# Performance work log

Measured on AMD Instinct MI355X. Metric: run time of the kernel, lower is better.

Reference implementation:

```python
import jax, jax.numpy as jnp
import numpy as np

B, L, D, H = 2, 2048, 1024, 16
DH = D // H
NEG = -10000.0

def setup_inputs() -> dict:
    key = jax.random.key(0)
    ks = jax.random.split(key, 6)
    scale = 1.0 / np.sqrt(D)
    inp = {
        "x": jax.random.normal(ks[0], (B, L, D), dtype=jnp.float32),
        "m": jnp.ones((B, L), dtype=jnp.int32),  # 1 = valid token, 0 = padded
        "Wq": jax.random.normal(ks[1], (D, D), dtype=jnp.float32) * scale,
        "bq": jnp.zeros((D,), dtype=jnp.float32),
        "Wk": jax.random.normal(ks[2], (D, D), dtype=jnp.float32) * scale,
        "bk": jnp.zeros((D,), dtype=jnp.float32),
        "Wv": jax.random.normal(ks[3], (D, D), dtype=jnp.float32) * scale,
        "bv": jnp.zeros((D,), dtype=jnp.float32),
        "Wp": jax.random.normal(ks[4], (D, D), dtype=jnp.float32) * scale,
        "bp": jnp.zeros((D,), dtype=jnp.float32),
    }
    return inp

def reference(x, m, Wq, bq, Wk, bk, Wv, bv, Wp, bp):
    # torch Linear: x @ W.T + b
    def heads(t):  # (B,L,D) -> (B,H,L,DH)
        return t.reshape(B, L, H, DH).transpose(0, 2, 1, 3)
    q = heads(x @ Wq.T + bq)
    k = heads(x @ Wk.T + bk)
    v = heads(x @ Wv.T + bv)
    att = jnp.einsum("bhqd,bhkd->bhqk", q, k) * (1.0 / np.sqrt(DH))  # (B,H,L,L)
    causal = jnp.tril(jnp.ones((L, L), dtype=bool))[None, None]       # (1,1,L,L)
    att = jnp.where(causal, att, NEG)
    # additive key-padding mask: 0 for valid, -10000 for padded keys
    pad = (1.0 - m.astype(att.dtype))[:, None, None, :] * NEG         # (B,1,1,L)
    att = att + pad
    att = jax.nn.softmax(att, axis=-1)
    y = jnp.einsum("bhqk,bhkd->bhqd", att, v)                          # (B,H,L,DH)
    y = y.transpose(0, 2, 1, 3).reshape(B, L, D)
    return y @ Wp.T + bp
```

## Files before the change

kernel.cpp:

```cpp
#include <hip/hip_runtime.h>
#include <hip/hip_bf16.h>

#define NB 2
#define NL 2048
#define ND 1024
#define NH 16
#define NDH 64
#define NM (NB*NL)

typedef unsigned short u16;
typedef __attribute__((ext_vector_type(8))) short short8;
typedef __attribute__((ext_vector_type(4))) float floatx4;

#define QSCALE 0.180336880f

__device__ __forceinline__ float bf2f(u16 u) {
  union { unsigned int ui; float f; } w;
  w.ui = ((unsigned int)u) << 16;
  return w.f;
}

__device__ __forceinline__ u16 f2bf(float f) {
  union { float f; unsigned int u; } v; v.f = f;
  unsigned int r = v.u + 0x7FFF + ((v.u >> 16) & 1);
  return (u16)(r >> 16);
}

__device__ __forceinline__ void async_cp16(const u16* lds, const u16* g) {
  __builtin_amdgcn_global_load_lds(
      (const __attribute__((address_space(1))) void*)g,
      (__attribute__((address_space(3))) void*)lds, 16, 0, 0);
}

__device__ __forceinline__ float dpp_xor1_f(float v) {
  return __int_as_float(__builtin_amdgcn_mov_dpp(__float_as_int(v), 0xB1, 0xF, 0xF, true));
}

__device__ __forceinline__ unsigned pk_bf16(float lo, float hi) {
  __hip_bfloat162 h2 = __float22bfloat162_rn(make_float2(lo, hi));
  return *(unsigned*)&h2;
}

__global__ __launch_bounds__(256)
void cvt_all(const float* __restrict__ wq, const float* __restrict__ wk,
             const float* __restrict__ wv, const float* __restrict__ wp,
             const float* __restrict__ x,
             u16* __restrict__ ow, u16* __restrict__ ox)
{
  const int per4 = ND * ND / 4;
  const int tot  = 4 * per4 + NM * ND / 4;
  for (int t = blockIdx.x * 256 + threadIdx.x; t < tot; t += gridDim.x * 256) {
    const float* src; uint2* dst; int off;
    if (t < 4 * per4) {
      int w = t >> 18; off = t & (per4 - 1);
      src = (w == 0) ? wq : (w == 1) ? wk : (w == 2) ? wv : wp;
      dst = (uint2*)(ow + (size_t)w * ND * ND);
    } else {
      off = t - 4 * per4; src = x; dst = (uint2*)ox;
    }
    float4 f = ((const float4*)src)[off];
    u16 h[4] = { f2bf(f.x), f2bf(f.y), f2bf(f.z), f2bf(f.w) };
    dst[off] = *(const uint2*)h;
  }
}

#define BM 128
#define BN 128
#define BK 32
#define LDT 32

__global__ __launch_bounds__(256)
void gemm_qkv(const u16* __restrict__ A, const u16* __restrict__ Wb,
              const float* __restrict__ bq, const float* __restrict__ bk,
              const float* __restrict__ bv,
              u16* __restrict__ Qb, u16* __restrict__ Kb, u16* __restrict__ Vb)
{
  const int n0g = blockIdx.x * BN;
  const int z   = n0g >> 10;
  const int n0  = n0g & 1023;
  const u16* W    = Wb + (size_t)z * ND * ND;
  const float* Bi = (z == 0) ? bq : (z == 1) ? bk : bv;
  u16* C          = (z == 0) ? Qb : (z == 1) ? Kb : Vb;
  const float sc  = (z == 0) ? QSCALE : 1.0f;

  const int m0 = blockIdx.y * BM;
  const int tid  = threadIdx.x;
  const int lane = tid & 63;
  const int wave = tid >> 6;
  const int wm = (wave >> 1) * 64;
  const int wn = (wave & 1) * 64;
  const int quad = lane >> 4;
  const int l16  = lane & 15;

  __shared__ u16 As[BM * LDT];
  __shared__ u16 Bs[BN * LDT];

  floatx4 acc[4][4];
#pragma unroll
  for (int i = 0; i < 4; ++i)
#pragma unroll
    for (int j = 0; j < 4; ++j)
      acc[i][j] = (floatx4){0.f, 0.f, 0.f, 0.f};

  for (int k0 = 0; k0 < ND; k0 += BK) {
#pragma unroll
    for (int it = 0; it < 2; ++it) {
      int idx = tid + it * 256;
      int rr  = idx >> 2;
      int c8  = (idx & 3) << 3;
      async_cp16(&Bs[idx * 8], &W[(size_t)(n0 + rr) * ND + k0 + c8]);
      async_cp16(&As[idx * 8], &A[(size_t)(m0 + rr) * ND + k0 + c8]);
    }
    __syncthreads();

    short8 af[4], bfr[4];
#pragma unroll
    for (int i = 0; i < 4; ++i)
      af[i] = *(const short8*)&As[(wm + i * 16 + l16) * LDT + quad * 8];
#pragma unroll
    for (int j = 0; j < 4; ++j)
      bfr[j] = *(const short8*)&Bs[(wn + j * 16 + l16) * LDT + quad * 8];

#pragma unroll
    for (int i = 0; i < 4; ++i)
#pragma unroll
      for (int j = 0; j < 4; ++j)
        acc[i][j] = __builtin_amdgcn_mfma_f32_16x16x32_bf16(af[i], bfr[j], acc[i][j], 0, 0, 0);
    __syncthreads();
  }

#pragma unroll
  for (int j = 0; j < 4; ++j) {
    const int ncol = n0 + wn + j * 16 + l16;
    const float bv2 = Bi[ncol];
#pragma unroll
    for (int i = 0; i < 4; ++i) {
      const int mbase = m0 + wm + i * 16 + quad * 4;
#pragma unroll
      for (int r2 = 0; r2 < 4; ++r2) {
        float v = (acc[i][j][r2] + bv2) * sc;
        C[(size_t)(mbase + r2) * ND + ncol] = f2bf(v);
      }
    }
  }
}

#define BN2 64

__global__ __launch_bounds__(256)
void gemm_proj(const u16* __restrict__ A, const u16* __restrict__ W,
               const float* __restrict__ Bi, float* __restrict__ C)
{
  const int n0 = blockIdx.x * BN2;
  const int m0 = blockIdx.y * BM;
  const int tid  = threadIdx.x;
  const int lane = tid & 63;
  const int wave = tid >> 6;
  const int wm = (wave >> 1) * 64;
  const int wn = (wave & 1) * 32;
  const int quad = lane >> 4;
  const int l16  = lane & 15;

  __shared__ u16 As[BM * LDT];
  __shared__ u16 Bs[BN2 * LDT];

  floatx4 acc[4][2];
#pragma unroll
  for (int i = 0; i < 4; ++i)
#pragma unroll
    for (int j = 0; j < 2; ++j)
      acc[i][j] = (floatx4){0.f, 0.f, 0.f, 0.f};

  for (int k0 = 0; k0 < ND; k0 += BK) {
#pragma unroll
    for (int it = 0; it < 2; ++it) {
      int idx = tid + it * 256;
      int rr  = idx >> 2;
      int c8  = (idx & 3) << 3;
      async_cp16(&As[idx * 8], &A[(size_t)(m0 + rr) * ND + k0 + c8]);
    }
    {
      int rr = tid >> 2, c8 = (tid & 3) << 3;
      async_cp16(&Bs[tid * 8], &W[(size_t)(n0 + rr) * ND + k0 + c8]);
    }
    __syncthreads();

    short8 af[4], bfr[2];
#pragma unroll
    for (int i = 0; i < 4; ++i)
      af[i] = *(const short8*)&As[(wm + i * 16 + l16) * LDT + quad * 8];
#pragma unroll
    for (int j = 0; j < 2; ++j)
      bfr[j] = *(const short8*)&Bs[(wn + j * 16 + l16) * LDT + quad * 8];

#pragma unroll
    for (int i = 0; i < 4; ++i)
#pragma unroll
      for (int j = 0; j < 2; ++j)
        acc[i][j] = __builtin_amdgcn_mfma_f32_16x16x32_bf16(af[i], bfr[j], acc[i][j], 0, 0, 0);
    __syncthreads();
  }

#pragma unroll
  for (int j = 0; j < 2; ++j) {
    const int ncol = n0 + wn + j * 16 + l16;
    const float bv2 = Bi[ncol];
#pragma unroll
    for (int i = 0; i < 4; ++i) {
      const int mbase = m0 + wm + i * 16 + quad * 4;
#pragma unroll
      for (int r2 = 0; r2 < 4; ++r2)
        C[(size_t)(mbase + r2) * ND + ncol] = acc[i][j][r2] + bv2;
    }
  }
}

#define TSTR 66
__global__ __launch_bounds__(256)
void vtrans(const u16* __restrict__ V, u16* __restrict__ VT)
{
  const int lt = blockIdx.x;
  const int bh = blockIdx.y;
  const int b = bh >> 4, h = bh & 15;
  const int l0 = lt * 64;
  const int tid = threadIdx.x;
  __shared__ u16 Ls[64][TSTR];
#pragma unroll
  for (int p = 0; p < 2; ++p) {
    int idx = tid + p * 256;
    int r = idx >> 3, c = (idx & 7) << 3;
    *(uint4*)&Ls[r][c] = *(const uint4*)&V[(size_t)(b * NL + l0 + r) * ND + h * NDH + c];
  }
  __syncthreads();
#pragma unroll
  for (int p = 0; p < 2; ++p) {
    int idx = tid + p * 256;
    int lg = idx & 7, d = idx >> 3;
    u16 tb[8];
#pragma unroll
    for (int e = 0; e < 8; ++e) tb[e] = Ls[lg * 8 + e][d];
    *(uint4*)&VT[((size_t)(b * NH + h) * NDH + d) * NL + l0 + lg * 8] = *(const uint4*)tb;
  }
}

#define KC 64
#define PSTR 72

__global__ __launch_bounds__(256)
void attn_mfma(const u16* __restrict__ Q, const u16* __restrict__ K,
               const u16* __restrict__ VT, const int* __restrict__ msk,
               u16* __restrict__ Y, u16* __restrict__ PO, float* __restrict__ PL)
{
  const int t = blockIdx.x;
  const int r = t >> 8;
  const int s = t & 255;
  const int xcd = s & 7;
  const int v = s >> 3;
  const int bh = xcd * 4 + (v & 3);
  const int p = v >> 2;

  int qt, kc_lo, half = 0;
  bool partial;
  if (r == 0)      { qt = p;      kc_lo = 0;           partial = false; }
  else if (r == 1) { qt = 15 - p; kc_lo = 0;           partial = false; }
  else if (r == 2) { qt = 16 + p; kc_lo = 0;           partial = true; half = 0; }
  else if (r == 3) { qt = 31 - p; kc_lo = (qt + 2) >> 1; partial = true; half = 1; }
  else if (r == 4) { qt = 31 - p; kc_lo = 0;           partial = true; half = 0; }
  else             { qt = 16 + p; kc_lo = (qt + 2) >> 1; partial = true; half = 1; }
  const int kc_hi = (partial && half == 0) ? ((qt + 2) >> 1) - 1 : qt;

  const int b = bh >> 4;
  const int h = bh & 15;
  const int q0 = qt * 64;
  const int tid  = threadIdx.x;
  const int lane = tid & 63;
  const int wave = tid >> 6;
  const int wq   = wave * 16;
  const int quad = lane >> 4;
  const int l16  = lane & 15;

  __shared__ u16 Ks[KC * 64];
  __shared__ u16 Vt[NDH * 64];
  __shared__ u16 Ps[64][PSTR];

  const u16* Kbase  = K  + (size_t)b * NL * ND + h * NDH;
  const u16* VTbase = VT + (size_t)(b * NH + h) * NDH * NL;
  const int* mbase  = msk + b * NL;

  short8 qf[2];
#pragma unroll
  for (int kk = 0; kk < 2; ++kk)
    qf[kk] = *(const short8*)&Q[(size_t)(b * NL + q0 + wq + l16) * ND
                                + h * NDH + kk * 32 + quad * 8];

  short8 onesf;
  {
    const short ov = (l16 == 0) ? (short)0x3F80 : (short)0;
#pragma unroll
    for (int e = 0; e < 8; ++e) onesf[e] = ov;
  }

  floatx4 o[4];
#pragma unroll
  for (int ot = 0; ot < 4; ++ot) o[ot] = (floatx4){0.f, 0.f, 0.f, 0.f};
  floatx4 lacc = (floatx4){0.f, 0.f, 0.f, 0.f};

  const int odd = l16 & 1;
  const int sw  = l16 & 7;
  const int rowb = q0 + wq + quad * 4;

  auto chunk_body = [&](int k0, bool diag) {
#pragma unroll
    for (int pp = 0; pp < 2; ++pp) {
      int sl = tid + pp * 256;
      int rr = sl >> 3;
      int ch = (sl & 7) ^ (rr & 7);
      async_cp16(&Ks[sl * 8], Kbase + (size_t)(k0 + rr) * ND + ch * 8);
      async_cp16(&Vt[sl * 8], VTbase + (size_t)rr * NL + k0 + ch * 8);
    }
    __syncthreads();

    int mm[4];
#pragma unroll
    for (int ct = 0; ct < 4; ++ct) mm[ct] = mbase[k0 + ct * 16 + l16];

    floatx4 sc4[4];
#pragma unroll
    for (int ct = 0; ct < 4; ++ct) {
      const u16* krow = &Ks[(ct * 16 + l16) * 64];
      short8 kf0 = *(const short8*)(krow + ((quad ^ sw) << 3));
      short8 kf1 = *(const short8*)(krow + (((4 | quad) ^ sw) << 3));
      floatx4 a = (floatx4){0.f, 0.f, 0.f, 0.f};
      a = __builtin_amdgcn_mfma_f32_16x16x32_bf16(qf[0], kf0, a, 0, 0, 0);
      a = __builtin_amdgcn_mfma_f32_16x16x32_bf16(qf[1], kf1, a, 0, 0, 0);
      sc4[ct] = a;
    }

#pragma unroll
    for (int ct = 0; ct < 4; ++ct) {
      const float pmul = (float)mm[ct];
      float pv[4];
#pragma unroll
      for (int r2 = 0; r2 < 4; ++r2) {
        float pr = pmul * __builtin_amdgcn_exp2f(sc4[ct][r2]);
        if (diag) {
          const int col = k0 + ct * 16 + l16;
          pr = (col > rowb + r2) ? 0.f : pr;
        }
        pv[r2] = pr;
      }
      float nb0 = dpp_xor1_f(pv[0]), nb1 = dpp_xor1_f(pv[1]);
      float nb2 = dpp_xor1_f(pv[2]), nb3 = dpp_xor1_f(pv[3]);
      const int colb  = ct * 16 + (l16 & ~1);
      const int row01 = wq + quad * 4 + odd;
      unsigned d01 = odd ? pk_bf16(nb1, pv[1]) : pk_bf16(pv[0], nb0);
      unsigned d23 = odd ? pk_bf16(nb3, pv[3]) : pk_bf16(pv[2], nb2);
      *(unsigned*)&Ps[row01][colb]     = d01;
      *(unsigned*)&Ps[row01 + 2][colb] = d23;
    }

#pragma unroll
    for (int kk = 0; kk < 2; ++kk) {
      short8 pf = *(const short8*)&Ps[wq + l16][kk * 32 + quad * 8];
#pragma unroll
      for (int ot = 0; ot < 4; ++ot) {
        const u16* vrow = &Vt[(ot * 16 + l16) * 64];
        short8 vf = *(const short8*)(vrow + ((((kk << 2) | quad) ^ sw) << 3));
        o[ot] = __builtin_amdgcn_mfma_f32_16x16x32_bf16(pf, vf, o[ot], 0, 0, 0);
      }
      lacc = __builtin_amdgcn_mfma_f32_16x16x32_bf16(pf, onesf, lacc, 0, 0, 0);
    }
    __syncthreads();
  };

  for (int kc = kc_lo; kc < kc_hi; ++kc) chunk_body(kc * KC, false);
  chunk_body(kc_hi * KC, kc_hi == qt);

  if (!partial) {
    float inv[4];
#pragma unroll
    for (int r2 = 0; r2 < 4; ++r2) {
      const float l = __shfl(lacc[r2], quad << 4);
      inv[r2] = 1.0f / l;
    }
#pragma unroll
    for (int ot = 0; ot < 4; ++ot)
#pragma unroll
      for (int r2 = 0; r2 < 4; ++r2) {
        const int row = q0 + wq + quad * 4 + r2;
        Y[(size_t)(b * NL + row) * ND + h * NDH + ot * 16 + l16] = f2bf(o[ot][r2] * inv[r2]);
      }
  } else {
    const int slot = (bh * 16 + (qt - 16)) * 2 + half;
    u16* po = PO + (size_t)slot * 4096;
#pragma unroll
    for (int ot = 0; ot < 4; ++ot)
#pragma unroll
      for (int r2 = 0; r2 < 4; ++r2)
        po[(wq + quad * 4 + r2) * 64 + ot * 16 + l16] = f2bf(o[ot][r2]);
    if (l16 == 0) {
#pragma unroll
      for (int r2 = 0; r2 < 4; ++r2)
        PL[slot * 64 + wq + quad * 4 + r2] = lacc[r2];
    }
  }
}

__global__ __launch_bounds__(256)
void attn_combine(const u16* __restrict__ PO, const float* __restrict__ PL,
                  u16* __restrict__ Y)
{
  const int tt = blockIdx.x;
  const int bh = tt >> 4, qx = tt & 15, qt = 16 + qx;
  const int b = bh >> 4, h = bh & 15;
  const int tid = threadIdx.x;
  const int row = tid >> 2, cg = (tid & 3) << 4;
  const int sl0 = (bh * 16 + qx) * 2;
  const float l = PL[sl0 * 64 + row] + PL[(sl0 + 1) * 64 + row];
  const float inv = 1.0f / l;
  const u16* p0 = PO + (size_t)sl0 * 4096 + row * 64 + cg;
  const u16* p1 = p0 + 4096;
  u16* y = Y + (size_t)(b * NL + qt * 64 + row) * ND + h * NDH + cg;
  uint4 a0 = *(const uint4*)p0, a1 = *(const uint4*)(p0 + 8);
  uint4 b0 = *(const uint4*)p1, b1 = *(const uint4*)(p1 + 8);
  const u16* ap = (const u16*)&a0; const u16* bp = (const u16*)&b0;
  u16 outv[16];
#pragma unroll
  for (int e = 0; e < 8; ++e) outv[e] = f2bf((bf2f(ap[e]) + bf2f(bp[e])) * inv);
  ap = (const u16*)&a1; bp = (const u16*)&b1;
#pragma unroll
  for (int e = 0; e < 8; ++e) outv[8 + e] = f2bf((bf2f(ap[e]) + bf2f(bp[e])) * inv);
  *(uint4*)y = *(const uint4*)outv;
  *(uint4*)(y + 8) = *(const uint4*)(outv + 8);
}

extern "C" void kernel_launch(void* const* d_in, const int* in_sizes, int n_in,
                              void* d_out, int out_size, void* d_ws, size_t ws_size,
                              hipStream_t stream) {
  const float* x  = (const float*)d_in[0];
  const int*   m  = (const int*)d_in[1];
  const float* Wq = (const float*)d_in[2];
  const float* bq = (const float*)d_in[3];
  const float* Wk = (const float*)d_in[4];
  const float* bk = (const float*)d_in[5];
  const float* Wv = (const float*)d_in[6];
  const float* bv = (const float*)d_in[7];
  const float* Wp = (const float*)d_in[8];
  const float* bp = (const float*)d_in[9];
  float* out = (float*)d_out;

  const size_t per = (size_t)NM * ND;
  u16* Qb = (u16*)d_ws;
  u16* Kb = Qb + per;
  u16* Vb = Kb + per;
  u16* Wb = Vb + per;
  u16* Yb = Qb;
  u16* xb = (u16*)d_out;
  u16* VTb = xb + per;
  u16* PO = xb;
  float* PL = (float*)Vb;

  cvt_all<<<2048, 256, 0, stream>>>(Wq, Wk, Wv, Wp, x, Wb, xb);

  gemm_qkv<<<dim3(3 * ND / BN, NM / BM), 256, 0, stream>>>(
      xb, Wb, bq, bk, bv, Qb, Kb, Vb);

  vtrans<<<dim3(NL / 64, NB * NH), 256, 0, stream>>>(Vb, VTb);

  attn_mfma<<<1536, 256, 0, stream>>>(Qb, Kb, VTb, m, Yb, PO, PL);

  attn_combine<<<512, 256, 0, stream>>>(PO, PL, Yb);

  const u16* Wpb = Wb + 3 * (size_t)ND * ND;
  gemm_proj<<<dim3(ND / BN2, NM / BM), 256, 0, stream>>>(Yb, Wpb, bp, out);
}
```

Measured before the change: 192.5 us.

## Rebalance causal attention work with table-driven 3-way key splits

Replaces the fixed six-round schedule with a constant lookup table that assigns each block a query tile and a key-chunk range. Tiles 10-21 are split into two partials and tiles 22-31 into three, giving 2048 more even blocks instead of 1536. Partial outputs are spread across two workspace regions, and the combine kernel now sums a variable number of partials. K and P now share one LDS buffer, which needs an extra barrier but lowers LDS use and may raise occupancy. The cost is more partial-write and combine traffic.

```diff
diff --git a/kernel.cpp b/kernel.cpp
--- a/kernel.cpp
+++ b/kernel.cpp
@@ -40,6 +40,26 @@
   __hip_bfloat162 h2 = __float22bfloat162_rn(make_float2(lo, hi));
   return *(unsigned*)&h2;
 }
+
+#define E(qt,lo,hi,p) ((unsigned)(qt) | ((unsigned)(lo)<<8) | ((unsigned)(hi)<<16) | ((unsigned)(p)<<24))
+__device__ __constant__ unsigned ATAB[64] = {
+  E(20,0,10,0), E(21,0,10,0), E(21,11,21,1), E(18,0,9,0),
+  E(16,0,8,0),  E(14,0,7,0),  E(10,6,10,1),  E(0,0,0,3),
+  E(30,0,10,0), E(31,0,10,0), E(31,11,21,1), E(19,0,9,0),
+  E(17,0,8,0),  E(15,0,7,0),  E(3,0,3,3),    E(1,0,1,3),
+  E(19,10,19,1), E(20,11,20,1), E(9,0,9,3),   E(17,9,17,1),
+  E(18,10,18,1), E(16,9,16,1),  E(13,0,6,0),  E(2,0,2,3),
+  E(27,0,9,0),  E(28,0,9,0),  E(28,10,19,1), E(8,0,8,3),
+  E(15,8,15,1), E(22,0,7,0),  E(11,0,5,0),   E(4,0,4,3),
+  E(29,0,9,0),  E(29,10,19,1), E(24,0,8,0),  E(25,0,8,0),
+  E(22,8,15,1), E(23,0,7,0),   E(11,6,11,1), E(12,7,12,1),
+  E(29,20,29,2), E(30,11,20,1), E(25,9,17,1), E(26,0,8,0),
+  E(23,8,15,1),  E(23,16,23,2), E(10,0,5,0),  E(5,0,5,3),
+  E(30,21,30,2), E(31,22,31,2), E(26,9,17,1), E(26,18,26,2),
+  E(13,7,13,1),  E(14,8,14,1),  E(6,0,6,3),   E(22,16,22,2),
+  E(27,10,18,1), E(27,19,27,2), E(28,20,28,2), E(24,9,16,1),
+  E(24,17,24,2), E(25,18,25,2), E(7,0,7,3),    E(12,0,6,0),
+};
 
 __global__ __launch_bounds__(256)
 void cvt_all(const float* __restrict__ wq, const float* __restrict__ wk,
@@ -249,7 +269,8 @@
 __global__ __launch_bounds__(256)
 void attn_mfma(const u16* __restrict__ Q, const u16* __restrict__ K,
                const u16* __restrict__ VT, const int* __restrict__ msk,
-               u16* __restrict__ Y, u16* __restrict__ PO, float* __restrict__ PL)
+               u16* __restrict__ Y, u16* __restrict__ PO0, u16* __restrict__ PO1,
+               float* __restrict__ PL)
 {
   const int t = blockIdx.x;
   const int r = t >> 8;
@@ -257,17 +278,13 @@
   const int xcd = s & 7;
   const int v = s >> 3;
   const int bh = xcd * 4 + (v & 3);
-  const int p = v >> 2;
-
-  int qt, kc_lo, half = 0;
-  bool partial;
-  if (r == 0)      { qt = p;      kc_lo = 0;           partial = false; }
-  else if (r == 1) { qt = 15 - p; kc_lo = 0;           partial = false; }
-  else if (r == 2) { qt = 16 + p; kc_lo = 0;           partial = true; half = 0; }
-  else if (r == 3) { qt = 31 - p; kc_lo = (qt + 2) >> 1; partial = true; half = 1; }
-  else if (r == 4) { qt = 31 - p; kc_lo = 0;           partial = true; half = 0; }
-  else             { qt = 16 + p; kc_lo = (qt + 2) >> 1; partial = true; half = 1; }
-  const int kc_hi = (partial && half == 0) ? ((qt + 2) >> 1) - 1 : qt;
+  const int g = v >> 2;
+
+  const unsigned e = ATAB[(g << 3) | r];
+  const int qt   = e & 255;
+  const int lo   = (e >> 8) & 255;
+  const int hi   = (e >> 16) & 255;
+  const int part = e >> 24;
 
   const int b = bh >> 4;
   const int h = bh & 15;
@@ -279,9 +296,8 @@
   const int quad = lane >> 4;
   const int l16  = lane & 15;
 
-  __shared__ u16 Ks[KC * 64];
+  __shared__ u16 KP[64 * PSTR];
   __shared__ u16 Vt[NDH * 64];
-  __shared__ u16 Ps[64][PSTR];
 
   const u16* Kbase  = K  + (size_t)b * NL * ND + h * NDH;
   const u16* VTbase = VT + (size_t)(b * NH + h) * NDH * NL;
@@ -297,7 +313,7 @@
   {
     const short ov = (l16 == 0) ? (short)0x3F80 : (short)0;
 #pragma unroll
-    for (int e = 0; e < 8; ++e) onesf[e] = ov;
+    for (int ee = 0; ee < 8; ++ee) onesf[ee] = ov;
   }
 
   floatx4 o[4];
@@ -315,7 +331,7 @@
       int sl = tid + pp * 256;
       int rr = sl >> 3;
       int ch = (sl & 7) ^ (rr & 7);
-      async_cp16(&Ks[sl * 8], Kbase + (size_t)(k0 + rr) * ND + ch * 8);
+      async_cp16(&KP[sl * 8], Kbase + (size_t)(k0 + rr) * ND + ch * 8);
       async_cp16(&Vt[sl * 8], VTbase + (size_t)rr * NL + k0 + ch * 8);
     }
     __syncthreads();
@@ -327,7 +343,7 @@
     floatx4 sc4[4];
 #pragma unroll
     for (int ct = 0; ct < 4; ++ct) {
-      const u16* krow = &Ks[(ct * 16 + l16) * 64];
+      const u16* krow = &KP[(ct * 16 + l16) * 64];
       short8 kf0 = *(const short8*)(krow + ((quad ^ sw) << 3));
       short8 kf1 = *(const short8*)(krow + (((4 | quad) ^ sw) << 3));
       floatx4 a = (floatx4){0.f, 0.f, 0.f, 0.f};
@@ -335,6 +351,7 @@
       a = __builtin_amdgcn_mfma_f32_16x16x32_bf16(qf[1], kf1, a, 0, 0, 0);
       sc4[ct] = a;
     }
+    __syncthreads();
 
 #pragma unroll
     for (int ct = 0; ct < 4; ++ct) {
@@ -355,13 +372,13 @@
       const int row01 = wq + quad * 4 + odd;
       unsigned d01 = odd ? pk_bf16(nb1, pv[1]) : pk_bf16(pv[0], nb0);
       unsigned d23 = odd ? pk_bf16(nb3, pv[3]) : pk_bf16(pv[2], nb2);
-      *(unsigned*)&Ps[row01][colb]     = d01;
-      *(unsigned*)&Ps[row01 + 2][colb] = d23;
+      *(unsigned*)&KP[row01 * PSTR + colb]       = d01;
+      *(unsigned*)&KP[(row01 + 2) * PSTR + colb] = d23;
     }
 
 #pragma unroll
     for (int kk = 0; kk < 2; ++kk) {
-      short8 pf = *(const short8*)&Ps[wq + l16][kk * 32 + quad * 8];
+      short8 pf = *(const short8*)&KP[(wq + l16) * PSTR + kk * 32 + quad * 8];
 #pragma unroll
       for (int ot = 0; ot < 4; ++ot) {
         const u16* vrow = &Vt[(ot * 16 + l16) * 64];
@@ -373,10 +390,10 @@
     __syncthreads();
   };
 
-  for (int kc = kc_lo; kc < kc_hi; ++kc) chunk_body(kc * KC, false);
-  chunk_body(kc_hi * KC, kc_hi == qt);
-
-  if (!partial) {
+  for (int kc = lo; kc < hi; ++kc) chunk_body(kc * KC, false);
+  chunk_body(hi * KC, hi == qt);
+
+  if (part == 3) {
     float inv[4];
 #pragma unroll
     for (int r2 = 0; r2 < 4; ++r2) {
@@ -391,8 +408,10 @@
         Y[(size_t)(b * NL + row) * ND + h * NDH + ot * 16 + l16] = f2bf(o[ot][r2] * inv[r2]);
       }
   } else {
-    const int slot = (bh * 16 + (qt - 16)) * 2 + half;
-    u16* po = PO + (size_t)slot * 4096;
+    const int base = (qt < 22) ? (qt - 10) * 2 : 24 + (qt - 22) * 3;
+    const int slot = bh * 54 + base + part;
+    u16* po = (slot < 1024) ? PO0 + (size_t)slot * 4096
+                            : PO1 + (size_t)(slot - 1024) * 4096;
 #pragma unroll
     for (int ot = 0; ot < 4; ++ot)
 #pragma unroll
@@ -407,29 +426,43 @@
 }
 
 __global__ __launch_bounds__(256)
-void attn_combine(const u16* __restrict__ PO, const float* __restrict__ PL,
-                  u16* __restrict__ Y)
+void attn_combine(const u16* __restrict__ PO0, const u16* __restrict__ PO1,
+                  const float* __restrict__ PL, u16* __restrict__ Y)
 {
   const int tt = blockIdx.x;
-  const int bh = tt >> 4, qx = tt & 15, qt = 16 + qx;
+  const int bh = tt / 22;
+  const int qt = 10 + (tt - bh * 22);
   const int b = bh >> 4, h = bh & 15;
   const int tid = threadIdx.x;
   const int row = tid >> 2, cg = (tid & 3) << 4;
-  const int sl0 = (bh * 16 + qx) * 2;
-  const float l = PL[sl0 * 64 + row] + PL[(sl0 + 1) * 64 + row];
+  const int nparts = (qt < 22) ? 2 : 3;
+  const int base = bh * 54 + ((qt < 22) ? (qt - 10) * 2 : 24 + (qt - 22) * 3);
+
+  float acc[16];
+#pragma unroll
+  for (int e = 0; e < 16; ++e) acc[e] = 0.f;
+  float l = 0.f;
+
+  for (int p = 0; p < nparts; ++p) {
+    const int slot = base + p;
+    const u16* po = (slot < 1024) ? PO0 + (size_t)slot * 4096
+                                  : PO1 + (size_t)(slot - 1024) * 4096;
+    const u16* src = po + row * 64 + cg;
+    uint4 a0 = *(const uint4*)src, a1 = *(const uint4*)(src + 8);
+    const u16* ap = (const u16*)&a0;
+#pragma unroll
+    for (int e = 0; e < 8; ++e) acc[e] += bf2f(ap[e]);
+    ap = (const u16*)&a1;
+#pragma unroll
+    for (int e = 0; e < 8; ++e) acc[8 + e] += bf2f(ap[e]);
+    l += PL[slot * 64 + row];
+  }
+
   const float inv = 1.0f / l;
-  const u16* p0 = PO + (size_t)sl0 * 4096 + row * 64 + cg;
-  const u16* p1 = p0 + 4096;
+  u16 outv[16];
+#pragma unroll
+  for (int e = 0; e < 16; ++e) outv[e] = f2bf(acc[e] * inv);
   u16* y = Y + (size_t)(b * NL + qt * 64 + row) * ND + h * NDH + cg;
-  uint4 a0 = *(const uint4*)p0, a1 = *(const uint4*)(p0 + 8);
-  uint4 b0 = *(const uint4*)p1, b1 = *(const uint4*)(p1 + 8);
-  const u16* ap = (const u16*)&a0; const u16* bp = (const u16*)&b0;
-  u16 outv[16];
-#pragma unroll
-  for (int e = 0; e < 8; ++e) outv[e] = f2bf((bf2f(ap[e]) + bf2f(bp[e])) * inv);
-  ap = (const u16*)&a1; bp = (const u16*)&b1;
-#pragma unroll
-  for (int e = 0; e < 8; ++e) outv[8 + e] = f2bf((bf2f(ap[e]) + bf2f(bp[e])) * inv);
   *(uint4*)y = *(const uint4*)outv;
   *(uint4*)(y + 8) = *(const uint4*)(outv + 8);
 }
@@ -457,8 +490,9 @@
   u16* Yb = Qb;
   u16* xb = (u16*)d_out;
   u16* VTb = xb + per;
-  u16* PO = xb;
-  float* PL = (float*)Vb;
+  u16* PO0 = xb;
+  u16* PO1 = Vb;
+  float* PL = (float*)(Vb + 3 * 1024 * 1024);
 
   cvt_all<<<2048, 256, 0, stream>>>(Wq, Wk, Wv, Wp, x, Wb, xb);
 
@@ -467,9 +501,9 @@
 
   vtrans<<<dim3(NL / 64, NB * NH), 256, 0, stream>>>(Vb, VTb);
 
-  attn_mfma<<<1536, 256, 0, stream>>>(Qb, Kb, VTb, m, Yb, PO, PL);
-
-  attn_combine<<<512, 256, 0, stream>>>(PO, PL, Yb);
+  attn_mfma<<<2048, 256, 0, stream>>>(Qb, Kb, VTb, m, Yb, PO0, PO1, PL);
+
+  attn_combine<<<704, 256, 0, stream>>>(PO0, PO1, PL, Yb);
 
   const u16* Wpb = Wb + 3 * (size_t)ND * ND;
   gemm_proj<<<dim3(ND / BN2, NM / BM), 256, 0, stream>>>(Yb, Wpb, bp, out);
```

Measured after the change: 195.5 us. About the same (+1.6%).

## Fuse V transpose into the QKV GEMM epilogue and drop the vtrans kernel

Applied to the files above, without the earlier changes.

For the V third of the QKV projection, the GEMM epilogue now stages the bf16 tile in shared memory transposed and writes it straight into the head-major VT layout. This removes the separate vtrans kernel, its launch, and the round trip of writing V and reading it back. In exchange, the GEMM block's shared-memory footprint roughly doubles to hold the transpose tile, which can reduce occupancy. The Q and K branches keep their original scalar-store epilogue.

```diff
diff --git a/kernel.cpp b/kernel.cpp
--- a/kernel.cpp
+++ b/kernel.cpp
@@ -68,19 +68,19 @@
 #define BN 128
 #define BK 32
 #define LDT 32
+#define TS 132
 
 __global__ __launch_bounds__(256)
 void gemm_qkv(const u16* __restrict__ A, const u16* __restrict__ Wb,
               const float* __restrict__ bq, const float* __restrict__ bk,
               const float* __restrict__ bv,
-              u16* __restrict__ Qb, u16* __restrict__ Kb, u16* __restrict__ Vb)
+              u16* __restrict__ Qb, u16* __restrict__ Kb, u16* __restrict__ VTb)
 {
   const int n0g = blockIdx.x * BN;
   const int z   = n0g >> 10;
   const int n0  = n0g & 1023;
   const u16* W    = Wb + (size_t)z * ND * ND;
   const float* Bi = (z == 0) ? bq : (z == 1) ? bk : bv;
-  u16* C          = (z == 0) ? Qb : (z == 1) ? Kb : Vb;
   const float sc  = (z == 0) ? QSCALE : 1.0f;
 
   const int m0 = blockIdx.y * BM;
@@ -92,8 +92,9 @@
   const int quad = lane >> 4;
   const int l16  = lane & 15;
 
-  __shared__ u16 As[BM * LDT];
-  __shared__ u16 Bs[BN * LDT];
+  __shared__ u16 SB[BM * TS];
+  u16* As = SB;
+  u16* Bs = SB + BM * LDT;
 
   floatx4 acc[4][4];
 #pragma unroll
@@ -129,17 +130,46 @@
     __syncthreads();
   }
 
-#pragma unroll
-  for (int j = 0; j < 4; ++j) {
-    const int ncol = n0 + wn + j * 16 + l16;
-    const float bv2 = Bi[ncol];
-#pragma unroll
-    for (int i = 0; i < 4; ++i) {
-      const int mbase = m0 + wm + i * 16 + quad * 4;
-#pragma unroll
-      for (int r2 = 0; r2 < 4; ++r2) {
-        float v = (acc[i][j][r2] + bv2) * sc;
-        C[(size_t)(mbase + r2) * ND + ncol] = f2bf(v);
+  if (z == 2) {
+#pragma unroll
+    for (int j = 0; j < 4; ++j) {
+      const int nl = wn + j * 16 + l16;
+      const float bv2 = Bi[n0 + nl];
+#pragma unroll
+      for (int i = 0; i < 4; ++i) {
+        const int ml = wm + i * 16 + quad * 4;
+        uint2 val;
+        val.x = pk_bf16(acc[i][j][0] + bv2, acc[i][j][1] + bv2);
+        val.y = pk_bf16(acc[i][j][2] + bv2, acc[i][j][3] + bv2);
+        *(uint2*)&SB[nl * TS + ml] = val;
+      }
+    }
+    __syncthreads();
+    const int b2 = m0 >> 11;
+    const int l0 = m0 & (NL - 1);
+#pragma unroll
+    for (int p = 0; p < 8; ++p) {
+      const int nl = p * 16 + (tid >> 4);
+      const int mc = (tid & 15) * 8;
+      const int ncol = n0 + nl;
+      const int h2 = ncol >> 6, d = ncol & 63;
+      uint4 v4 = *(const uint4*)&SB[nl * TS + mc];
+      *(uint4*)&VTb[((size_t)(b2 * NH + h2) * NDH + d) * NL + l0 + mc] = v4;
+    }
+  } else {
+    u16* C = (z == 0) ? Qb : Kb;
+#pragma unroll
+    for (int j = 0; j < 4; ++j) {
+      const int ncol = n0 + wn + j * 16 + l16;
+      const float bv2 = Bi[ncol];
+#pragma unroll
+      for (int i = 0; i < 4; ++i) {
+        const int mbase = m0 + wm + i * 16 + quad * 4;
+#pragma unroll
+        for (int r2 = 0; r2 < 4; ++r2) {
+          float v = (acc[i][j][r2] + bv2) * sc;
+          C[(size_t)(mbase + r2) * ND + ncol] = f2bf(v);
+        }
       }
     }
   }
@@ -215,34 +245,6 @@
   }
 }
 
-#define TSTR 66
-__global__ __launch_bounds__(256)
-void vtrans(const u16* __restrict__ V, u16* __restrict__ VT)
-{
-  const int lt = blockIdx.x;
-  const int bh = blockIdx.y;
-  const int b = bh >> 4, h = bh & 15;
-  const int l0 = lt * 64;
-  const int tid = threadIdx.x;
-  __shared__ u16 Ls[64][TSTR];
-#pragma unroll
-  for (int p = 0; p < 2; ++p) {
-    int idx = tid + p * 256;
-    int r = idx >> 3, c = (idx & 7) << 3;
-    *(uint4*)&Ls[r][c] = *(const uint4*)&V[(size_t)(b * NL + l0 + r) * ND + h * NDH + c];
-  }
-  __syncthreads();
-#pragma unroll
-  for (int p = 0; p < 2; ++p) {
-    int idx = tid + p * 256;
-    int lg = idx & 7, d = idx >> 3;
-    u16 tb[8];
-#pragma unroll
-    for (int e = 0; e < 8; ++e) tb[e] = Ls[lg * 8 + e][d];
-    *(uint4*)&VT[((size_t)(b * NH + h) * NDH + d) * NL + l0 + lg * 8] = *(const uint4*)tb;
-  }
-}
-
 #define KC 64
 #define PSTR 72
 
@@ -297,7 +299,7 @@
   {
     const short ov = (l16 == 0) ? (short)0x3F80 : (short)0;
 #pragma unroll
-    for (int e = 0; e < 8; ++e) onesf[e] = ov;
+    for (int ee = 0; ee < 8; ++ee) onesf[ee] = ov;
   }
 
   floatx4 o[4];
@@ -463,9 +465,7 @@
   cvt_all<<<2048, 256, 0, stream>>>(Wq, Wk, Wv, Wp, x, Wb, xb);
 
   gemm_qkv<<<dim3(3 * ND / BN, NM / BM), 256, 0, stream>>>(
-      xb, Wb, bq, bk, bv, Qb, Kb, Vb);
-
-  vtrans<<<dim3(NL / 64, NB * NH), 256, 0, stream>>>(Vb, VTb);
+      xb, Wb, bq, bk, bv, Qb, Kb, VTb);
 
   attn_mfma<<<1536, 256, 0, stream>>>(Qb, Kb, VTb, m, Yb, PO, PL);
 
```

Result: slower. 201.8 us (+4.8%).
